# Kernel optimization log

Measured on AMD Instinct MI355X. Metric: run time of the kernel, lower is better.

## Reference

```python
import jax, jax.numpy as jnp
import numpy as np

B, C, H = 2, 32, 64  # batch, concat channels, cube side (H==W==D required by attaxis reshapes)
Ch = C // 2


def _conv3d(x, w, b, pad):
    # conv3d block = Conv3d + bias + ReLU (n=1 conv block)
    y = jax.lax.conv_general_dilated(x, w, (1, 1, 1), [(p, p) for p in pad],
                                     dimension_numbers=('NCDHW', 'OIDHW', 'NCDHW'))
    return jax.nn.relu(y + b[None, :, None, None, None])


def setup_inputs():
    key = jax.random.key(0)
    ks = jax.random.split(key, 16)
    w = lambda k, s: jax.random.normal(k, s, dtype=jnp.float32) * 0.05
    z = lambda n: jnp.zeros((n,), jnp.float32)
    return {
        'x1': jax.random.normal(ks[0], (B, Ch, H, H, H), jnp.float32),
        'x2': jax.random.normal(ks[1], (B, Ch, H, H, H), jnp.float32),
        'w_red': w(ks[2], (1, C, 3, 3, 3)), 'b_red': z(1),
        'w_cx': w(ks[3], (1, 1, 1, 1, H)), 'b_cx': z(1),
        'w_cy': w(ks[4], (1, 1, 1, H, 1)), 'b_cy': z(1),
        'w_cz': w(ks[5], (1, 1, H, 1, 1)), 'b_cz': z(1),
        'w_sp1': w(ks[6], (1, 1, 1, 1, 1)), 'b_sp1': z(1),
        'w_sp3': w(ks[7], (1, 1, 3, 3, 3)), 'b_sp3': z(1),
        'w_sp5a': w(ks[8], (1, 1, 3, 3, 3)), 'b_sp5a': z(1),
        'w_sp5b': w(ks[9], (1, 1, 3, 3, 3)), 'b_sp5b': z(1),
        'w_fus': w(ks[10], (C, 1, 3, 3, 3)), 'b_fus': z(C),
        'w_c1': w(ks[11], (Ch, Ch, 3, 3, 3)), 'b_c1': z(Ch),
        'w_c2': w(ks[12], (Ch, Ch, 3, 3, 3)), 'b_c2': z(Ch),
    }


def _kernal(x, w_cx, b_cx, w_cy, b_cy, w_cz, b_cz,
            w_sp1, b_sp1, w_sp3, b_sp3, w_sp5a, b_sp5a, w_sp5b, b_sp5b):
    b, c, h, ww, d = x.shape
    # xyzaxis: axis-collapsing convs, then attaxis attention over S = h*w tokens
    q = _conv3d(x, w_cx, b_cx, (0, 0, 0))                        # [b,1,h,w,1]
    k = jnp.swapaxes(_conv3d(x, w_cy, b_cy, (0, 0, 0)), 3, 4)    # [b,1,h,d,1]
    v = jnp.swapaxes(_conv3d(x, w_cz, b_cz, (0, 0, 0)), 2, 4)    # [b,1,d,w,1]
    S = h * ww
    Q = q.reshape(b, S, 1)
    K = k.reshape(b, S, 1)
    V = v.reshape(b, S, 1)
    qk = jax.nn.softmax(jnp.einsum('bsc,btc->bst', Q, K), axis=-1)  # [b,S,S]
    xyz = jnp.einsum('bst,btc->bsc', qk, V).reshape(b, 1, h, ww, 1)
    # multi-branch convs + full-tensor att(sp1, sp3, sp5)
    sp1 = _conv3d(x, w_sp1, b_sp1, (0, 0, 0))
    sp3 = _conv3d(x, w_sp3, b_sp3, (1, 1, 1))
    sp5 = _conv3d(_conv3d(x, w_sp5a, b_sp5a, (1, 1, 1)), w_sp5b, b_sp5b, (1, 1, 1))
    attn = jnp.matmul(jax.nn.softmax(jnp.matmul(sp1, sp3), axis=-1), sp5)
    return xyz + attn + x  # xyz broadcasts over last dim


def reference(x1, x2, w_red, b_red, w_cx, b_cx, w_cy, b_cy, w_cz, b_cz,
              w_sp1, b_sp1, w_sp3, b_sp3, w_sp5a, b_sp5a, w_sp5b, b_sp5b,
              w_fus, b_fus, w_c1, b_c1, w_c2, b_c2):
    x = jnp.concatenate([x1, x2], axis=1)                 # [B,C,H,H,H]
    hx = _conv3d(x, w_red, b_red, (1, 1, 1))              # DenseSP.reducePool -> 1 channel
    hx = _kernal(hx, w_cx, b_cx, w_cy, b_cy, w_cz, b_cz,
                 w_sp1, b_sp1, w_sp3, b_sp3, w_sp5a, b_sp5a, w_sp5b, b_sp5b)
    sp = jax.nn.sigmoid(_conv3d(hx, w_fus, b_fus, (1, 1, 1)) + x)  # DenseSP output
    x = sp * x + x
    c = x.shape[1] // 2
    y1 = _conv3d(x[:, :c] + x1, w_c1, b_c1, (1, 1, 1))
    y2 = _conv3d(x[:, c:] + x2, w_c2, b_c2, (1, 1, 1))
    return (y1, y2)
```

## Files before the change

### kernel.cpp

```cpp
#include <hip/hip_runtime.h>

#define DEVFN static __device__ __forceinline__

constexpr int HHH = 262144;
constexpr int HH  = 4096;

typedef __attribute__((ext_vector_type(8))) short short8;
typedef __attribute__((ext_vector_type(4))) float f32x4;

#define OFF_HX   ((size_t)0)
#define OFF_SP3  (OFF_HX   + 2*(size_t)HHH)
#define OFF_SP5A (OFF_SP3  + 2*(size_t)HHH)
#define OFF_SP5B (OFF_SP5A + 2*(size_t)HHH)
#define OFF_HXO  (OFF_SP5B + 2*(size_t)HHH)
#define OFF_Q    (OFF_HXO  + 2*(size_t)HHH)
#define OFF_K    (OFF_Q    + 2*(size_t)HH)
#define OFF_V    (OFF_K    + 2*(size_t)HH)
#define OFF_XYZ  (OFF_V    + 2*(size_t)HH)
#define OFF_KM   (OFF_XYZ  + 2*(size_t)HH)
#define OFF_Z    (OFF_KM   + 16)
#define OFF_WPRE (OFF_Z    + 32*(size_t)HHH)

DEVFN unsigned short f2bf(float f)
{
    unsigned u = __builtin_bit_cast(unsigned, f);
    u += 0x7fffu + ((u >> 16) & 1u);
    return (unsigned short)(u >> 16);
}

DEVFN void stage1800(const float* __restrict__ src, float* __restrict__ tile,
                     int z0, int y0, int x0, int tid)
{
    for (int i = tid; i < 1800; i += 256) {
        int lz = i / 180;
        int r  = i - lz * 180;
        int ly = r / 18;
        int lx = r - ly * 18;
        int gz = z0 - 1 + lz, gy = y0 - 1 + ly, gx = x0 - 1 + lx;
        float v = 0.f;
        if ((unsigned)(gz | gy | gx) < 64u)
            v = src[(gz * 64 + gy) * 64 + gx];
        tile[i] = v;
    }
}

DEVFN float4 conv27(const float* __restrict__ tile, int tz, int ty, int txg,
                    const float* __restrict__ wc, float4 acc)
{
#pragma unroll
    for (int dz = 0; dz < 3; ++dz) {
#pragma unroll
        for (int dy = 0; dy < 3; ++dy) {
            const float2* row = (const float2*)&tile[((tz + dz) * 10 + (ty + dy)) * 18 + txg * 4];
            float2 p0 = row[0], p1 = row[1], p2 = row[2];
            const float* wr = wc + (dz * 3 + dy) * 3;
            float w0 = wr[0], w1 = wr[1], w2 = wr[2];
            acc.x = fmaf(p0.x, w0, fmaf(p0.y, w1, fmaf(p1.x, w2, acc.x)));
            acc.y = fmaf(p0.y, w0, fmaf(p1.x, w1, fmaf(p1.y, w2, acc.y)));
            acc.z = fmaf(p1.x, w0, fmaf(p1.y, w1, fmaf(p2.x, w2, acc.z)));
            acc.w = fmaf(p1.y, w0, fmaf(p2.x, w1, fmaf(p2.y, w2, acc.w)));
        }
    }
    return acc;
}

__global__ __launch_bounds__(256) void k_wprep(
    const float* __restrict__ w1, const float* __restrict__ w2,
    unsigned short* __restrict__ wpre)
{
    int item = blockIdx.x * 256 + threadIdx.x;
    if (item >= 1792) return;
    int half = item / 896;
    int rem  = item - half * 896;
    int t = rem >> 6, lane = rem & 63;
    const float* w = half ? w2 : w1;
    int co = lane & 15, g = lane >> 4;
    int cihalf = g & 1, tapsel = g >> 1;
    int tap = 2 * t + tapsel;
    unsigned v[4] = {0u, 0u, 0u, 0u};
    if (tap < 27) {
#pragma unroll
        for (int p = 0; p < 4; ++p) {
            unsigned short lo = f2bf(w[(co * 16 + cihalf * 8 + 2 * p) * 27 + tap]);
            unsigned short hi = f2bf(w[(co * 16 + cihalf * 8 + 2 * p + 1) * 27 + tap]);
            v[p] = (unsigned)lo | ((unsigned)hi << 16);
        }
    }
    uint4 pk = {v[0], v[1], v[2], v[3]};
    ((uint4*)wpre)[item] = pk;
}

__global__ __launch_bounds__(256) void k_conv_red32(
    const float* __restrict__ x1, const float* __restrict__ x2,
    const float* __restrict__ w, const float* __restrict__ bias,
    float* __restrict__ hx)
{
    __shared__ __align__(16) float buf[2][1080];
    const int tid = threadIdx.x;
    const int tz = tid >> 6, ty = (tid >> 3) & 7, tx2 = tid & 7;
    const int bz = blockIdx.z;
    const int b = bz >> 4, z0 = (bz & 15) * 4;
    const int y0 = blockIdx.y * 8, x0 = blockIdx.x * 16;

    int gofs[5];
    bool inb[5];
#pragma unroll
    for (int k = 0; k < 5; ++k) {
        int i = tid + k * 256;
        inb[k] = false; gofs[k] = 0;
        if (i < 1080) {
            int lz = i / 180, r = i - lz * 180, ly = r / 18, lx = r - ly * 18;
            int gz = z0 - 1 + lz, gy = y0 - 1 + ly, gx = x0 - 1 + lx;
            if ((unsigned)(gz | gy | gx) < 64u) {
                inb[k] = true;
                gofs[k] = (gz * 64 + gy) * 64 + gx;
            }
        }
    }

    {
        const float* s = x1 + (size_t)(b * 16) * HHH;
#pragma unroll
        for (int k = 0; k < 5; ++k) {
            int i = tid + k * 256;
            if (i < 1080) buf[0][i] = inb[k] ? s[gofs[k]] : 0.f;
        }
    }
    __syncthreads();

    float2 acc = {0.f, 0.f};
    for (int c = 0; c < 32; ++c) {
        float r[5];
        if (c < 31) {
            int cn = c + 1;
            const float* s = (cn < 16 ? x1 : x2) + (size_t)(b * 16 + (cn & 15)) * HHH;
#pragma unroll
            for (int k = 0; k < 5; ++k)
                r[k] = inb[k] ? s[gofs[k]] : 0.f;
        }
        const float* wc = w + c * 27;
        const float* tb = buf[c & 1];
#pragma unroll
        for (int dz = 0; dz < 3; ++dz) {
#pragma unroll
            for (int dy = 0; dy < 3; ++dy) {
                const float2* row = (const float2*)&tb[((tz + dz) * 10 + (ty + dy)) * 18 + tx2 * 2];
                float2 p0 = row[0], p1 = row[1];
                const float* wr = wc + (dz * 3 + dy) * 3;
                float w0 = wr[0], w1 = wr[1], w2 = wr[2];
                acc.x = fmaf(p0.x, w0, fmaf(p0.y, w1, fmaf(p1.x, w2, acc.x)));
                acc.y = fmaf(p0.y, w0, fmaf(p1.x, w1, fmaf(p1.y, w2, acc.y)));
            }
        }
        if (c < 31) {
#pragma unroll
            for (int k = 0; k < 5; ++k) {
                int i = tid + k * 256;
                if (i < 1080) buf[(c + 1) & 1][i] = r[k];
            }
        }
        __syncthreads();
    }
    float bv = bias[0];
    float2 o = {fmaxf(acc.x + bv, 0.f), fmaxf(acc.y + bv, 0.f)};
    size_t oidx = (size_t)b * HHH + ((size_t)(z0 + tz) * 64 + (y0 + ty)) * 64 + (x0 + tx2 * 2);
    *(float2*)&hx[oidx] = o;
}

__global__ __launch_bounds__(256) void k_conv1ch(
    const float* __restrict__ in, const float* __restrict__ w,
    const float* __restrict__ bias, float* __restrict__ outp)
{
    __shared__ __align__(16) float tile[1800];
    const int tid = threadIdx.x;
    const int tz = tid >> 5, ty = (tid >> 2) & 7, txg = tid & 3;
    const int b  = blockIdx.z >> 3;
    const int z0 = (blockIdx.z & 7) * 8, y0 = blockIdx.y * 8, x0 = blockIdx.x * 16;

    stage1800(in + (size_t)b * HHH, tile, z0, y0, x0, tid);
    __syncthreads();
    float4 acc = {0.f, 0.f, 0.f, 0.f};
    acc = conv27(tile, tz, ty, txg, w, acc);
    float bv = bias[0];
    float4 o = {fmaxf(acc.x + bv, 0.f), fmaxf(acc.y + bv, 0.f),
                fmaxf(acc.z + bv, 0.f), fmaxf(acc.w + bv, 0.f)};
    size_t oidx = (size_t)b * HHH + ((size_t)(z0 + tz) * 64 + (y0 + ty)) * 64 + (x0 + txg * 4);
    *(float4*)&outp[oidx] = o;
}

__global__ __launch_bounds__(256) void k_conv1ch_dual(
    const float* __restrict__ in,
    const float* __restrict__ wa, const float* __restrict__ ba, float* __restrict__ oa,
    const float* __restrict__ wb, const float* __restrict__ bb, float* __restrict__ ob)
{
    __shared__ __align__(16) float tile[1800];
    const int tid = threadIdx.x;
    const int tz = tid >> 5, ty = (tid >> 2) & 7, txg = tid & 3;
    const int b  = blockIdx.z >> 3;
    const int z0 = (blockIdx.z & 7) * 8, y0 = blockIdx.y * 8, x0 = blockIdx.x * 16;

    stage1800(in + (size_t)b * HHH, tile, z0, y0, x0, tid);
    __syncthreads();
    float4 zero = {0.f, 0.f, 0.f, 0.f};
    float4 aA = conv27(tile, tz, ty, txg, wa, zero);
    float4 aB = conv27(tile, tz, ty, txg, wb, zero);
    float bva = ba[0], bvb = bb[0];
    float4 ra = {fmaxf(aA.x + bva, 0.f), fmaxf(aA.y + bva, 0.f),
                 fmaxf(aA.z + bva, 0.f), fmaxf(aA.w + bva, 0.f)};
    float4 rb = {fmaxf(aB.x + bvb, 0.f), fmaxf(aB.y + bvb, 0.f),
                 fmaxf(aB.z + bvb, 0.f), fmaxf(aB.w + bvb, 0.f)};
    size_t oidx = (size_t)b * HHH + ((size_t)(z0 + tz) * 64 + (y0 + ty)) * 64 + (x0 + txg * 4);
    *(float4*)&oa[oidx] = ra;
    *(float4*)&ob[oidx] = rb;
}

__global__ __launch_bounds__(256) void k_qk(
    const float* __restrict__ hx,
    const float* __restrict__ wq, const float* __restrict__ bq,
    const float* __restrict__ wk, const float* __restrict__ bk,
    float* __restrict__ Q, float* __restrict__ K)
{
    const int bi = blockIdx.x;
    const float* src = hx + (size_t)bi * HH;
    const int tid = threadIdx.x;
    const int j = tid >> 2, q = tid & 3;

    float a = 0.f;
    const float4* sv = (const float4*)(src + j * 64 + q * 16);
#pragma unroll
    for (int k = 0; k < 4; ++k) {
        float4 vv = sv[k];
        a = fmaf(vv.x, wq[q * 16 + k * 4 + 0], a);
        a = fmaf(vv.y, wq[q * 16 + k * 4 + 1], a);
        a = fmaf(vv.z, wq[q * 16 + k * 4 + 2], a);
        a = fmaf(vv.w, wq[q * 16 + k * 4 + 3], a);
    }
    a += __shfl_xor(a, 1); a += __shfl_xor(a, 2);

    float c = 0.f;
#pragma unroll
    for (int jj = 0; jj < 16; ++jj)
        c = fmaf(src[(q * 16 + jj) * 64 + j], wk[q * 16 + jj], c);
    c += __shfl_xor(c, 1); c += __shfl_xor(c, 2);

    if (q == 0) {
        Q[(size_t)bi * 64 + j] = fmaxf(a + bq[0], 0.f);
        K[(size_t)bi * 64 + j] = fmaxf(c + bk[0], 0.f);
    }
}

__global__ __launch_bounds__(256) void k_v(
    const float* __restrict__ hx, const float* __restrict__ wv,
    const float* __restrict__ bv, float* __restrict__ V)
{
    const int bt = blockIdx.x;
    const int b = bt >> 6, t = bt & 63;
    const int tid = threadIdx.x;
    const int j = tid >> 2, q = tid & 3;
    const float* src = hx + (size_t)b * HHH + (size_t)j * 64 + t;
    float a = 0.f;
#pragma unroll
    for (int k = 0; k < 16; ++k) {
        int i = q * 16 + k;
        a = fmaf(src[(size_t)i * HH], wv[i], a);
    }
    a += __shfl_xor(a, 1); a += __shfl_xor(a, 2);
    if (q == 0)
        V[(size_t)b * HH + t * 64 + j] = fmaxf(a + bv[0], 0.f);
}

__global__ void k_kmax(const float* __restrict__ K, float* __restrict__ kmax)
{
    __shared__ float red[256];
    int b = blockIdx.x;
    float m = -1e30f;
    for (int u = threadIdx.x; u < 4096; u += 256) m = fmaxf(m, K[b * 4096 + u]);
    red[threadIdx.x] = m;
    __syncthreads();
    for (int s = 128; s > 0; s >>= 1) {
        if (threadIdx.x < s) red[threadIdx.x] = fmaxf(red[threadIdx.x], red[threadIdx.x + s]);
        __syncthreads();
    }
    if (threadIdx.x == 0) kmax[b] = red[0];
}

__global__ __launch_bounds__(256) void k_xyz(
    const float* __restrict__ Q, const float* __restrict__ K,
    const float* __restrict__ V, const float* __restrict__ kmax,
    float* __restrict__ xyz)
{
    __shared__ float pden[4][64];
    __shared__ float pnum[4][64];
    const int b = blockIdx.y;
    const int chunk = blockIdx.x;
    const int lane = threadIdx.x & 63;
    const int wv = __builtin_amdgcn_readfirstlane(threadIdx.x >> 6);
    const int s = chunk * 64 + lane;
    const float qv = Q[b * 4096 + s];
    const float m = qv * kmax[b];
    const float* Kp = K + b * 4096 + wv * 1024;
    const float* Vp = V + b * 4096 + wv * 1024;
    float den = 0.f, num = 0.f;
#pragma unroll 4
    for (int u = 0; u < 1024; ++u) {
        float e = __expf(fmaf(qv, Kp[u], -m));
        den += e;
        num = fmaf(e, Vp[u], num);
    }
    pden[wv][lane] = den;
    pnum[wv][lane] = num;
    __syncthreads();
    if (threadIdx.x < 64) {
        float d = pden[0][lane] + pden[1][lane] + pden[2][lane] + pden[3][lane];
        float n = pnum[0][lane] + pnum[1][lane] + pnum[2][lane] + pnum[3][lane];
        xyz[b * 4096 + s] = n / d;
    }
}

DEVFN void mac16(const float4* __restrict__ base, int vb, float a, float* acc)
{
    float4 q0 = base[vb], q1 = base[vb + 1], q2 = base[vb + 2], q3 = base[vb + 3];
    float qq[16] = {q0.x, q0.y, q0.z, q0.w, q1.x, q1.y, q1.z, q1.w,
                    q2.x, q2.y, q2.z, q2.w, q3.x, q3.y, q3.z, q3.w};
#pragma unroll
    for (int k = 0; k < 16; ++k) acc[k] = fmaf(a, qq[k], acc[k]);
}

__global__ __launch_bounds__(256) void k_attn(
    const float* __restrict__ hx, const float* __restrict__ sp3,
    const float* __restrict__ sp5, const float* __restrict__ xyz,
    const float* __restrict__ w_sp1, const float* __restrict__ b_sp1,
    float* __restrict__ hxo)
{
    __shared__ __align__(16) float s1[64 * 65];
    __shared__ __align__(16) float s3[4096];
    __shared__ __align__(16) float s5[4096];
    const int tid = threadIdx.x;
    const int bi = blockIdx.x;
    const size_t off = (size_t)bi * HH;
    const float w1 = w_sp1[0], bb = b_sp1[0];
    for (int idx = tid; idx < 4096; idx += 256) {
        float hv = hx[off + idx];
        s1[(idx >> 6) * 65 + (idx & 63)] = fmaxf(fmaf(w1, hv, bb), 0.f);
        s3[idx] = sp3[off + idx];
        s5[idx] = sp5[off + idx];
    }
    __syncthreads();
    const int j = tid >> 2, g = tid & 3, t0 = g * 16;
    float m[16];
#pragma unroll
    for (int k = 0; k < 16; ++k) m[k] = 0.f;
    const float4* s3v = (const float4*)s3;
    for (int r = 0; r < 64; ++r) {
        float a = s1[j * 65 + r];
        mac16(s3v, r * 16 + (t0 >> 2), a, m);
    }
    float mx = m[0];
#pragma unroll
    for (int k = 1; k < 16; ++k) mx = fmaxf(mx, m[k]);
    mx = fmaxf(mx, __shfl_xor(mx, 1));
    mx = fmaxf(mx, __shfl_xor(mx, 2));
    float e[16];
    float sum = 0.f;
#pragma unroll
    for (int k = 0; k < 16; ++k) { e[k] = __expf(m[k] - mx); sum += e[k]; }
    sum += __shfl_xor(sum, 1);
    sum += __shfl_xor(sum, 2);
    const float inv = 1.f / sum;
    __syncthreads();
#pragma unroll
    for (int k = 0; k < 16; ++k) s1[j * 65 + t0 + k] = e[k] * inv;
    __syncthreads();
    float acc[16];
#pragma unroll
    for (int k = 0; k < 16; ++k) acc[k] = 0.f;
    const float4* s5v = (const float4*)s5;
    for (int r = 0; r < 64; ++r) {
        float a = s1[j * 65 + r];
        mac16(s5v, r * 16 + (t0 >> 2), a, acc);
    }
    const float xv = xyz[(size_t)(bi >> 6) * HH + (size_t)(bi & 63) * 64 + j];
    const size_t ob = off + (size_t)j * 64 + t0;
#pragma unroll
    for (int k = 0; k < 16; ++k)
        hxo[ob + k] = xv + acc[k] + hx[ob + k];
}

DEVFN float zcalc(float gg, float bf, float xv)
{
    float t = fmaxf(gg + bf, 0.f) + xv;
    float s = 1.f / (1.f + __expf(-t));
    return xv * (s + 2.f);
}

__global__ __launch_bounds__(256) void k_fuse_half(
    const float* __restrict__ hxo, const float* __restrict__ x1,
    const float* __restrict__ x2, const float* __restrict__ w_fus,
    const float* __restrict__ b_fus, unsigned short* __restrict__ Zb)
{
    __shared__ __align__(16) float tile[1800];
    const int tid = threadIdx.x;
    const int tz = tid >> 5, ty = (tid >> 2) & 7, txg = tid & 3;
    const int bz = blockIdx.z;
    const int zt = bz & 7, bh = bz >> 3;
    const int b = bh >> 1, half = bh & 1;
    const int z0 = zt * 8, y0 = blockIdx.y * 8, x0 = blockIdx.x * 16;

    stage1800(hxo + (size_t)b * HHH, tile, z0, y0, x0, tid);
    __syncthreads();

    const size_t vox = ((size_t)(z0 + tz) * 64 + (y0 + ty)) * 64 + (x0 + txg * 4);
    const float* xbase = (half ? x2 : x1) + (size_t)(b * 16) * HHH + vox;
    const float* wbase = w_fus + (half * 16) * 27;
    const float* bbase = b_fus + half * 16;

    unsigned zp[4][8];
#pragma unroll
    for (int cc = 0; cc < 16; ++cc) {
        float4 g = {0.f, 0.f, 0.f, 0.f};
        g = conv27(tile, tz, ty, txg, wbase + cc * 27, g);
        float4 xv = *(const float4*)(xbase + (size_t)cc * HHH);
        float bf = bbase[cc];
        unsigned short z0v = f2bf(zcalc(g.x, bf, xv.x));
        unsigned short z1v = f2bf(zcalc(g.y, bf, xv.y));
        unsigned short z2v = f2bf(zcalc(g.z, bf, xv.z));
        unsigned short z3v = f2bf(zcalc(g.w, bf, xv.w));
        int p = cc >> 1;
        if ((cc & 1) == 0) {
            zp[0][p] = z0v; zp[1][p] = z1v; zp[2][p] = z2v; zp[3][p] = z3v;
        } else {
            zp[0][p] |= (unsigned)z0v << 16; zp[1][p] |= (unsigned)z1v << 16;
            zp[2][p] |= (unsigned)z2v << 16; zp[3][p] |= (unsigned)z3v << 16;
        }
    }
    unsigned short* zo = Zb + ((size_t)bh * HHH + vox) * 16;
#pragma unroll
    for (int v = 0; v < 4; ++v) {
        uint4 lo = {zp[v][0], zp[v][1], zp[v][2], zp[v][3]};
        uint4 hi = {zp[v][4], zp[v][5], zp[v][6], zp[v][7]};
        *(uint4*)(zo + v * 16)     = lo;
        *(uint4*)(zo + v * 16 + 8) = hi;
    }
}

__global__ __launch_bounds__(512) void k_convc_mfma(
    const unsigned short* __restrict__ Zb,
    const unsigned short* __restrict__ wpre,
    const float* __restrict__ b1, const float* __restrict__ b2,
    float* __restrict__ out)
{
    __shared__ __align__(16) unsigned short tile[1800 * 16];
    const int tid = threadIdx.x;
    const int lane = tid & 63;
    const int wvid = tid >> 6;
    const int bz = blockIdx.z;
    const int b = bz >> 4, half = (bz >> 3) & 1, z0 = (bz & 7) * 8;
    const int y0 = blockIdx.y * 8, x0 = blockIdx.x * 16;
    const float* bias = half ? b2 : b1;

    const int g = lane >> 4;
    const int cihalf = g & 1;
    const int tapsel = g >> 1;

    short8 wf[14];
    const short8* wp = (const short8*)wpre + (half * 14) * 64 + lane;
#pragma unroll
    for (int t = 0; t < 14; ++t) wf[t] = wp[t * 64];

    float bfrag[4];
#pragma unroll
    for (int r = 0; r < 4; ++r) bfrag[r] = bias[g * 4 + r];

    const unsigned short* zsrc = Zb + (size_t)(b * 2 + half) * HHH * 16;
    for (int i = tid; i < 3600; i += 512) {
        int pos = i >> 1, h = i & 1;
        int lz = pos / 180;
        int r2 = pos - lz * 180;
        int ly = r2 / 18, lx = r2 - ly * 18;
        int gz = z0 - 1 + lz, gy = y0 - 1 + ly, gx = x0 - 1 + lx;
        uint4 pk = {0u, 0u, 0u, 0u};
        if ((unsigned)(gz | gy | gx) < 64u) {
            size_t gvox = ((size_t)(gz * 64 + gy)) * 64 + gx;
            pk = *(const uint4*)(zsrc + gvox * 16 + h * 8);
        }
        *(uint4*)&tile[pos * 16 + h * 8] = pk;
    }
    __syncthreads();

    int offs[14];
#pragma unroll
    for (int t = 0; t < 14; ++t) {
        int tap = 2 * t + tapsel;
        int tcl = tap < 27 ? tap : 26;
        int dz = tcl / 9, rr = tcl - dz * 9;
        int dy = rr / 3, dx = rr - dy * 3;
        offs[t] = (((dz * 10 + dy) * 18 + dx + (lane & 15)) << 5) + (cihalf << 4);
    }

    const char* tb = (const char*)tile;
    for (int rr = 0; rr < 8; ++rr) {
        int rowid = wvid * 8 + rr;
        int zr = rowid >> 3, yr = rowid & 7;
        int rbase = ((zr * 10 + yr) * 18) << 5;
        f32x4 acc = {0.f, 0.f, 0.f, 0.f};
        f32x4 acc2 = {0.f, 0.f, 0.f, 0.f};
#pragma unroll
        for (int t = 0; t < 14; t += 2) {
            short8 bf0 = *(const short8*)(tb + (rbase + offs[t]));
            acc = __builtin_amdgcn_mfma_f32_16x16x32_bf16(wf[t], bf0, acc, 0, 0, 0);
            short8 bf1 = *(const short8*)(tb + (rbase + offs[t + 1]));
            acc2 = __builtin_amdgcn_mfma_f32_16x16x32_bf16(wf[t + 1], bf1, acc2, 0, 0, 0);
        }
        size_t vox = ((size_t)(z0 + zr) * 64 + (y0 + yr)) * 64 + x0 + (lane & 15);
        float* ob = out + (size_t)half * (2 * 16 * (size_t)HHH) + (size_t)(b * 16) * HHH + vox;
#pragma unroll
        for (int r = 0; r < 4; ++r) {
            float v = acc[r] + acc2[r] + bfrag[r];
            ob[(size_t)(g * 4 + r) * HHH] = fmaxf(v, 0.f);
        }
    }
}

extern "C" void kernel_launch(void* const* d_in, const int* in_sizes, int n_in,
                              void* d_out, int out_size, void* d_ws, size_t ws_size,
                              hipStream_t stream)
{
    const float* x1     = (const float*)d_in[0];
    const float* x2     = (const float*)d_in[1];
    const float* w_red  = (const float*)d_in[2];
    const float* b_red  = (const float*)d_in[3];
    const float* w_cx   = (const float*)d_in[4];
    const float* b_cx   = (const float*)d_in[5];
    const float* w_cy   = (const float*)d_in[6];
    const float* b_cy   = (const float*)d_in[7];
    const float* w_cz   = (const float*)d_in[8];
    const float* b_cz   = (const float*)d_in[9];
    const float* w_sp1  = (const float*)d_in[10];
    const float* b_sp1  = (const float*)d_in[11];
    const float* w_sp3  = (const float*)d_in[12];
    const float* b_sp3  = (const float*)d_in[13];
    const float* w_sp5a = (const float*)d_in[14];
    const float* b_sp5a = (const float*)d_in[15];
    const float* w_sp5b = (const float*)d_in[16];
    const float* b_sp5b = (const float*)d_in[17];
    const float* w_fus  = (const float*)d_in[18];
    const float* b_fus  = (const float*)d_in[19];
    const float* w_c1   = (const float*)d_in[20];
    const float* b_c1   = (const float*)d_in[21];
    const float* w_c2   = (const float*)d_in[22];
    const float* b_c2   = (const float*)d_in[23];

    float* ws  = (float*)d_ws;
    float* out = (float*)d_out;

    float* HX   = ws + OFF_HX;
    float* SP3  = ws + OFF_SP3;
    float* SP5A = ws + OFF_SP5A;
    float* SP5B = ws + OFF_SP5B;
    float* HXO  = ws + OFF_HXO;
    float* Qb   = ws + OFF_Q;
    float* Kb   = ws + OFF_K;
    float* Vb   = ws + OFF_V;
    float* XYZb = ws + OFF_XYZ;
    float* KM   = ws + OFF_KM;
    unsigned short* Zb   = (unsigned short*)(ws + OFF_Z);
    unsigned short* WPRE = (unsigned short*)(ws + OFF_WPRE);

    k_wprep    <<<7, 256, 0, stream>>>(w_c1, w_c2, WPRE);
    k_conv_red32<<<dim3(4, 8, 32), 256, 0, stream>>>(x1, x2, w_red, b_red, HX);
    k_conv1ch_dual<<<dim3(4, 8, 16), 256, 0, stream>>>(HX, w_sp3, b_sp3, SP3,
                                                       w_sp5a, b_sp5a, SP5A);
    k_conv1ch  <<<dim3(4, 8, 16), 256, 0, stream>>>(SP5A, w_sp5b, b_sp5b, SP5B);
    k_qk       <<<128, 256, 0, stream>>>(HX, w_cx, b_cx, w_cy, b_cy, Qb, Kb);
    k_v        <<<128, 256, 0, stream>>>(HX, w_cz, b_cz, Vb);
    k_kmax     <<<2, 256, 0, stream>>>(Kb, KM);
    k_xyz      <<<dim3(64, 2), 256, 0, stream>>>(Qb, Kb, Vb, KM, XYZb);
    k_attn     <<<128, 256, 0, stream>>>(HX, SP3, SP5B, XYZb, w_sp1, b_sp1, HXO);
    k_fuse_half<<<dim3(4, 8, 32), 256, 0, stream>>>(HXO, x1, x2, w_fus, b_fus, Zb);
    k_convc_mfma<<<dim3(4, 8, 32), 512, 0, stream>>>(Zb, WPRE, b_c1, b_c2, out);
}
```

Baseline: 206.5 us.

## Pad LDS row pitch to 19 and triple-buffer channel staging in reduce conv

Changes the shared-memory tile row pitch from 18 to 19 floats across the 1-channel conv stencils, so row accesses land on different LDS banks. The loads become scalar instead of float2 as a result. The 32-channel reduction conv also moves from double to triple buffering, with register prefetch two channels ahead, so global load latency overlaps more compute. The cost is more scalar LDS instructions, more registers and slightly larger shared arrays.

```diff
diff --git a/kernel.cpp b/kernel.cpp
--- a/kernel.cpp
+++ b/kernel.cpp
@@ -4,6 +4,7 @@
 
 constexpr int HHH = 262144;
 constexpr int HH  = 4096;
+constexpr int RP  = 19;
 
 typedef __attribute__((ext_vector_type(8))) short short8;
 typedef __attribute__((ext_vector_type(4))) float f32x4;
@@ -40,7 +41,7 @@
         float v = 0.f;
         if ((unsigned)(gz | gy | gx) < 64u)
             v = src[(gz * 64 + gy) * 64 + gx];
-        tile[i] = v;
+        tile[(lz * 10 + ly) * RP + lx] = v;
     }
 }
 
@@ -51,14 +52,15 @@
     for (int dz = 0; dz < 3; ++dz) {
 #pragma unroll
         for (int dy = 0; dy < 3; ++dy) {
-            const float2* row = (const float2*)&tile[((tz + dz) * 10 + (ty + dy)) * 18 + txg * 4];
-            float2 p0 = row[0], p1 = row[1], p2 = row[2];
+            const float* row = &tile[((tz + dz) * 10 + (ty + dy)) * RP + txg * 4];
+            float p0 = row[0], p1 = row[1], p2 = row[2];
+            float p3 = row[3], p4 = row[4], p5 = row[5];
             const float* wr = wc + (dz * 3 + dy) * 3;
             float w0 = wr[0], w1 = wr[1], w2 = wr[2];
-            acc.x = fmaf(p0.x, w0, fmaf(p0.y, w1, fmaf(p1.x, w2, acc.x)));
-            acc.y = fmaf(p0.y, w0, fmaf(p1.x, w1, fmaf(p1.y, w2, acc.y)));
-            acc.z = fmaf(p1.x, w0, fmaf(p1.y, w1, fmaf(p2.x, w2, acc.z)));
-            acc.w = fmaf(p1.y, w0, fmaf(p2.x, w1, fmaf(p2.y, w2, acc.w)));
+            acc.x = fmaf(p0, w0, fmaf(p1, w1, fmaf(p2, w2, acc.x)));
+            acc.y = fmaf(p1, w0, fmaf(p2, w1, fmaf(p3, w2, acc.y)));
+            acc.z = fmaf(p2, w0, fmaf(p3, w1, fmaf(p4, w2, acc.z)));
+            acc.w = fmaf(p3, w0, fmaf(p4, w1, fmaf(p5, w2, acc.w)));
         }
     }
     return acc;
@@ -95,21 +97,23 @@
     const float* __restrict__ w, const float* __restrict__ bias,
     float* __restrict__ hx)
 {
-    __shared__ __align__(16) float buf[2][1080];
+    __shared__ __align__(16) float buf[3][1140];
     const int tid = threadIdx.x;
     const int tz = tid >> 6, ty = (tid >> 3) & 7, tx2 = tid & 7;
     const int bz = blockIdx.z;
     const int b = bz >> 4, z0 = (bz & 15) * 4;
     const int y0 = blockIdx.y * 8, x0 = blockIdx.x * 16;
 
-    int gofs[5];
-    bool inb[5];
+    int gofs[5], lidx[5];
+    bool inb[5], act[5];
 #pragma unroll
     for (int k = 0; k < 5; ++k) {
         int i = tid + k * 256;
-        inb[k] = false; gofs[k] = 0;
-        if (i < 1080) {
+        act[k] = (i < 1080);
+        inb[k] = false; gofs[k] = 0; lidx[k] = 0;
+        if (act[k]) {
             int lz = i / 180, r = i - lz * 180, ly = r / 18, lx = r - ly * 18;
+            lidx[k] = (lz * 10 + ly) * RP + lx;
             int gz = z0 - 1 + lz, gy = y0 - 1 + ly, gx = x0 - 1 + lx;
             if ((unsigned)(gz | gy | gx) < 64u) {
                 inb[k] = true;
@@ -118,49 +122,54 @@
         }
     }
 
-    {
-        const float* s = x1 + (size_t)(b * 16) * HHH;
-#pragma unroll
-        for (int k = 0; k < 5; ++k) {
-            int i = tid + k * 256;
-            if (i < 1080) buf[0][i] = inb[k] ? s[gofs[k]] : 0.f;
-        }
-    }
+#define LOADCH(c, rdst)                                                         \
+    {                                                                           \
+        const float* s_ = ((c) < 16 ? x1 : x2) + (size_t)(b * 16 + ((c) & 15)) * HHH; \
+        _Pragma("unroll")                                                       \
+        for (int k = 0; k < 5; ++k) rdst[k] = (act[k] && inb[k]) ? s_[gofs[k]] : 0.f; \
+    }
+#define STORECH(buf_, rsrc)                                                     \
+    {                                                                           \
+        _Pragma("unroll")                                                       \
+        for (int k = 0; k < 5; ++k) if (act[k]) (buf_)[lidx[k]] = rsrc[k];      \
+    }
+
+    float rcur[5], rnext[5];
+    LOADCH(0, rcur);
+    STORECH(buf[0], rcur);
+    LOADCH(1, rcur);
     __syncthreads();
 
     float2 acc = {0.f, 0.f};
+    int cur = 0;
     for (int c = 0; c < 32; ++c) {
-        float r[5];
-        if (c < 31) {
-            int cn = c + 1;
-            const float* s = (cn < 16 ? x1 : x2) + (size_t)(b * 16 + (cn & 15)) * HHH;
-#pragma unroll
-            for (int k = 0; k < 5; ++k)
-                r[k] = inb[k] ? s[gofs[k]] : 0.f;
-        }
+        if (c + 2 < 32) LOADCH(c + 2, rnext);
         const float* wc = w + c * 27;
-        const float* tb = buf[c & 1];
+        const float* tb = buf[cur];
 #pragma unroll
         for (int dz = 0; dz < 3; ++dz) {
 #pragma unroll
             for (int dy = 0; dy < 3; ++dy) {
-                const float2* row = (const float2*)&tb[((tz + dz) * 10 + (ty + dy)) * 18 + tx2 * 2];
-                float2 p0 = row[0], p1 = row[1];
+                const float* row = &tb[((tz + dz) * 10 + (ty + dy)) * RP + tx2 * 2];
+                float p0 = row[0], p1 = row[1], p2 = row[2], p3 = row[3];
                 const float* wr = wc + (dz * 3 + dy) * 3;
                 float w0 = wr[0], w1 = wr[1], w2 = wr[2];
-                acc.x = fmaf(p0.x, w0, fmaf(p0.y, w1, fmaf(p1.x, w2, acc.x)));
-                acc.y = fmaf(p0.y, w0, fmaf(p1.x, w1, fmaf(p1.y, w2, acc.y)));
+                acc.x = fmaf(p0, w0, fmaf(p1, w1, fmaf(p2, w2, acc.x)));
+                acc.y = fmaf(p1, w0, fmaf(p2, w1, fmaf(p3, w2, acc.y)));
             }
         }
-        if (c < 31) {
-#pragma unroll
-            for (int k = 0; k < 5; ++k) {
-                int i = tid + k * 256;
-                if (i < 1080) buf[(c + 1) & 1][i] = r[k];
-            }
-        }
+        int nxt = cur == 2 ? 0 : cur + 1;
+        if (c + 1 < 32) {
+            STORECH(buf[nxt], rcur);
+#pragma unroll
+            for (int k = 0; k < 5; ++k) rcur[k] = rnext[k];
+        }
+        cur = nxt;
         __syncthreads();
     }
+#undef LOADCH
+#undef STORECH
+
     float bv = bias[0];
     float2 o = {fmaxf(acc.x + bv, 0.f), fmaxf(acc.y + bv, 0.f)};
     size_t oidx = (size_t)b * HHH + ((size_t)(z0 + tz) * 64 + (y0 + ty)) * 64 + (x0 + tx2 * 2);
@@ -171,7 +180,7 @@
     const float* __restrict__ in, const float* __restrict__ w,
     const float* __restrict__ bias, float* __restrict__ outp)
 {
-    __shared__ __align__(16) float tile[1800];
+    __shared__ __align__(16) float tile[1900];
     const int tid = threadIdx.x;
     const int tz = tid >> 5, ty = (tid >> 2) & 7, txg = tid & 3;
     const int b  = blockIdx.z >> 3;
@@ -193,7 +202,7 @@
     const float* __restrict__ wa, const float* __restrict__ ba, float* __restrict__ oa,
     const float* __restrict__ wb, const float* __restrict__ bb, float* __restrict__ ob)
 {
-    __shared__ __align__(16) float tile[1800];
+    __shared__ __align__(16) float tile[1900];
     const int tid = threadIdx.x;
     const int tz = tid >> 5, ty = (tid >> 2) & 7, txg = tid & 3;
     const int b  = blockIdx.z >> 3;
@@ -398,7 +407,7 @@
     const float* __restrict__ x2, const float* __restrict__ w_fus,
     const float* __restrict__ b_fus, unsigned short* __restrict__ Zb)
 {
-    __shared__ __align__(16) float tile[1800];
+    __shared__ __align__(16) float tile[1900];
     const int tid = threadIdx.x;
     const int tz = tid >> 5, ty = (tid >> 2) & 7, txg = tid & 3;
     const int bz = blockIdx.z;
```

Result: no change. 205.2 us (-0.6%).
